# Optimization experiments

Measured on AMD Instinct MI355X. Metric: run time of the kernel, lower is better.

## Reference

```python
import jax, jax.numpy as jnp
import numpy as np

PRED, TOTAL, ITEM = 100000, 120000, 100000
NUI = PRED + ITEM            # nodes in user2item / reverse-consumption graphs
NODES = TOTAL + ITEM         # embedding table rows
EMB = 64
EPS = 1e-5


def _gatv2(src, dst, x, Wl, bl, Wr, br, attn, n):
    """DGL GATv2Conv (1 head), activation=leaky_relu(0.01)."""
    fs = x @ Wl + bl                                   # fc_src
    fd = x @ Wr + br                                   # fc_dst
    e = jax.nn.leaky_relu(fs[src] + fd[dst], 0.2) @ attn   # [E_edges]
    m = jax.ops.segment_max(e, dst, n)                 # per-dst max (stable softmax)
    ex = jnp.exp(e - m[dst])
    denom = jax.ops.segment_sum(ex, dst, n)
    alpha = ex / denom[dst]                            # edge softmax over in-edges
    out = jax.ops.segment_sum(alpha[:, None] * fs[src], dst, n)
    return jax.nn.leaky_relu(out, 0.01)


def _bn(x, g, b):
    mu = jnp.mean(x, 0)
    var = jnp.var(x, 0)
    return (x - mu) * jax.lax.rsqrt(var + EPS) * g + b


def _mlp(x, W, b, g, beta):
    # Linear -> BatchNorm1d (train mode, batch stats) -> LeakyReLU(0.01)
    return jax.nn.leaky_relu(_bn(x @ W + b, g, beta), 0.01)


def _cheb(src, dst, x, W, b, lam, n):
    """ChebConv order-3: h = sum_k T_k(Lhat) x @ W_k + b, leaky_relu."""
    deg = jnp.clip(jax.ops.segment_sum(jnp.ones_like(dst, jnp.float32), dst, n), 1.0)
    dinv = jax.lax.rsqrt(deg)
    norm = dinv[src] * dinv[dst]                       # D^-1/2 A D^-1/2 edge weight

    def lhat(v):  # (2/lam)(I - Ahat) v - v
        av = jax.ops.segment_sum(norm[:, None] * v[src], dst, n)
        return (2.0 / lam) * (v - av) - v

    T0 = x
    T1 = lhat(T0)
    T2 = 2.0 * lhat(T1) - T0
    return jax.nn.leaky_relu(T0 @ W[0] + T1 @ W[1] + T2 @ W[2] + b, 0.01)


def setup_inputs() -> dict:
    key = jax.random.key(0)
    ks = jax.random.split(key, 24)
    ri = lambda k, n, hi: jax.random.randint(k, (n,), 0, hi, dtype=jnp.int32)
    rn = lambda k, shp, s=0.1: jax.random.normal(k, shp, jnp.float32) * s
    return {
        "emb": rn(ks[0], (NODES, EMB), 1.0),
        "bn0_g": jnp.ones((EMB,), jnp.float32),
        "bn0_b": jnp.zeros((EMB,), jnp.float32),
        "gat_Wl": rn(ks[1], (5, EMB, EMB)),
        "gat_bl": jnp.zeros((5, EMB), jnp.float32),
        "gat_Wr": rn(ks[2], (5, EMB, EMB)),
        "gat_br": jnp.zeros((5, EMB), jnp.float32),
        "gat_attn": rn(ks[3], (5, EMB)),
        "cheb_W": rn(ks[4], (3, EMB, EMB)),
        "cheb_b": jnp.zeros((EMB,), jnp.float32),
        "mlp_W": rn(ks[5], (5, 2 * EMB, EMB)),
        "mlp_b": jnp.zeros((5, EMB), jnp.float32),
        "mlp_g": jnp.ones((5, EMB), jnp.float32),
        "mlp_beta": jnp.zeros((5, EMB), jnp.float32),
        "lambda_max": jnp.array([2.0], jnp.float32),
        "u2i_src": ri(ks[6], 1500000, NUI),
        "u2i_dst": ri(ks[7], 1500000, NUI),
        "rc_src": ri(ks[8], 1500000, NUI),
        "rc_dst": ri(ks[9], 1500000, NUI),
        "i2u_src": ri(ks[10], 1000000, PRED),
        "i2u_dst": ri(ks[11], 1000000, PRED),
        "i2u_ids": jnp.arange(PRED, dtype=jnp.int32),
        "sn_src": ri(ks[12], 1000000, PRED),
        "sn_dst": ri(ks[13], 1000000, PRED),
        "snn_src": ri(ks[14], 1500000, TOTAL),
        "snn_dst": ri(ks[15], 1500000, TOTAL),
    }


def reference(emb, bn0_g, bn0_b, gat_Wl, gat_bl, gat_Wr, gat_br, gat_attn,
              cheb_W, cheb_b, mlp_W, mlp_b, mlp_g, mlp_beta, lambda_max,
              u2i_src, u2i_dst, rc_src, rc_dst, i2u_src, i2u_dst, i2u_ids,
              sn_src, sn_dst, snn_src, snn_dst):
    gat = lambda i, src, dst, x, n: _gatv2(src, dst, x, gat_Wl[i], gat_bl[i],
                                           gat_Wr[i], gat_br[i], gat_attn[i], n)
    mlp = lambda i, x: _mlp(x, mlp_W[i], mlp_b[i], mlp_g[i], mlp_beta[i])

    e = _bn(emb, bn0_g, bn0_b)                        # embedding_BN over all nodes
    pred_u = e[:PRED]
    total_u = e[:TOTAL]
    item_e = e[-ITEM:]
    uie = jnp.concatenate([pred_u, item_e], axis=0)   # [NUI, EMB]

    # --- spatial attention: item influence branch ---
    u2i_emb = gat(0, u2i_src, u2i_dst, uie, NUI)
    iie = gat(1, rc_src, rc_dst, u2i_emb, NUI)[:PRED]

    # --- spatial attention: social item branch ---
    su = uie[i2u_ids]                                 # embedding[_ID]
    i2u_emb = gat(2, i2u_src, i2u_dst, su, PRED)
    soc = uie[:PRED]                                  # embedding[social_g.nodes()]
    mask = (jnp.sum(i2u_emb, axis=1) != 0)[:, None]
    soc = soc.at[i2u_ids].set(jnp.where(mask, i2u_emb, soc[i2u_ids]))
    sie = gat(3, sn_src, sn_dst, soc, PRED)

    user_item_embed = mlp(0, jnp.concatenate([iie, sie], axis=1))

    # --- spectral attention ---
    lam = lambda_max[0]
    h = _cheb(snn_src, snn_dst, total_u, cheb_W, cheb_b, lam, TOTAL)
    h = _cheb(snn_src, snn_dst, h, cheb_W, cheb_b, lam, TOTAL)
    user_social_embed = gat(4, snn_src, snn_dst, h, TOTAL)[:PRED]

    # --- mutualistic layer ---
    h_uP = mlp(1, jnp.concatenate([user_item_embed, pred_u], axis=1))
    h_uS = mlp(2, jnp.concatenate([user_social_embed, pred_u], axis=1))
    h_m = h_uP * h_uS
    h_mP = jnp.concatenate([h_m * jax.nn.softmax(h_uP, axis=1), h_uP], axis=1)
    h_mS = jnp.concatenate([h_m * jax.nn.softmax(h_uS, axis=1), h_uS], axis=1)

    # --- prediction layer ---
    h_new_P = mlp(3, h_mP)
    h_new_S = mlp(4, h_mS)
    return (h_new_P, h_new_S)
```

## Files before the change

kernel.cpp:

```cpp
#include <hip/hip_runtime.h>
#include <math.h>

static const int PRED  = 100000;
static const int TOTAL = 120000;
static const int ITEM  = 100000;
static const int NUI   = PRED + ITEM;
static const int NODES = TOTAL + ITEM;
#define BN_EPS 1e-5f

__device__ inline float lrelu(float v, float s) { return v > 0.f ? v : s * v; }

__global__ void k_bn_stats(const float* __restrict__ x, int n, float* __restrict__ sums) {
  __shared__ float ls[256], ls2[256];
  int t = threadIdx.x;
  int col = t & 63;
  float s = 0.f, s2 = 0.f;
  for (int r = blockIdx.x * 4 + (t >> 6); r < n; r += gridDim.x * 4) {
    float v = x[(size_t)r * 64 + col];
    s += v; s2 += v * v;
  }
  ls[t] = s; ls2[t] = s2;
  __syncthreads();
  if (t < 64) {
    atomicAdd(&sums[t],      ls[t] + ls[t + 64] + ls[t + 128] + ls[t + 192]);
    atomicAdd(&sums[64 + t], ls2[t] + ls2[t + 64] + ls2[t + 128] + ls2[t + 192]);
  }
}

__global__ void k_bn_apply(const float* __restrict__ x, float* __restrict__ y,
                           const float* __restrict__ sums,
                           const float* __restrict__ g, const float* __restrict__ b,
                           int n, int relu) {
  size_t tot4 = (size_t)n * 16;
  size_t i = (size_t)blockIdx.x * blockDim.x + threadIdx.x;
  size_t st = (size_t)gridDim.x * blockDim.x;
  float inv_n = 1.f / (float)n;
  const float4* x4 = (const float4*)x;
  float4* y4 = (float4*)y;
  for (; i < tot4; i += st) {
    int c4 = (int)(i & 15) * 4;
    float4 v = x4[i];
    float4 o;
    #pragma unroll
    for (int j = 0; j < 4; ++j) {
      int c = c4 + j;
      float mean = sums[c] * inv_n;
      float var = fmaxf(sums[64 + c] * inv_n - mean * mean, 0.f);
      float vv = (j == 0) ? v.x : (j == 1) ? v.y : (j == 2) ? v.z : v.w;
      float oo = (vv - mean) * rsqrtf(var + BN_EPS) * g[c] + b[c];
      if (relu) oo = lrelu(oo, 0.01f);
      if (j == 0) o.x = oo; else if (j == 1) o.y = oo; else if (j == 2) o.z = oo; else o.w = oo;
    }
    y4[i] = o;
  }
}

__global__ void k_bn0_apply(const float* __restrict__ x, float* __restrict__ e_tot,
                            float* __restrict__ uie, const float* __restrict__ sums,
                            const float* __restrict__ g, const float* __restrict__ b) {
  size_t tot4 = (size_t)NODES * 16;
  size_t i = (size_t)blockIdx.x * blockDim.x + threadIdx.x;
  size_t st = (size_t)gridDim.x * blockDim.x;
  float inv_n = 1.f / (float)NODES;
  const float4* x4 = (const float4*)x;
  float4* e4 = (float4*)e_tot;
  float4* u4 = (float4*)uie;
  for (; i < tot4; i += st) {
    int c4 = (int)(i & 15) * 4;
    size_t row = i >> 4;
    float4 v = x4[i];
    float4 o;
    #pragma unroll
    for (int j = 0; j < 4; ++j) {
      int c = c4 + j;
      float mean = sums[c] * inv_n;
      float var = fmaxf(sums[64 + c] * inv_n - mean * mean, 0.f);
      float vv = (j == 0) ? v.x : (j == 1) ? v.y : (j == 2) ? v.z : v.w;
      float oo = (vv - mean) * rsqrtf(var + BN_EPS) * g[c] + b[c];
      if (j == 0) o.x = oo; else if (j == 1) o.y = oo; else if (j == 2) o.z = oo; else o.w = oo;
    }
    if (row < (size_t)TOTAL) e4[i] = o;
    else u4[((row - TOTAL) + PRED) * 16 + (i & 15)] = o;
    if (row < (size_t)PRED) u4[i] = o;
  }
}

__global__ __launch_bounds__(256) void k_gemm_dual(const float* __restrict__ A,
    const float* __restrict__ Wl, const float* __restrict__ bl,
    const float* __restrict__ Wr, const float* __restrict__ br,
    float* __restrict__ FS, float* __restrict__ FD, int n) {
  __shared__ float As[128][65];
  __shared__ float Ws[64][68];
  int t = threadIdx.x;
  int row0 = blockIdx.x * 128;
  for (int i = t; i < 2048; i += 256) {
    int r = i >> 4, c = (i & 15) * 4, gr = row0 + r;
    float4 a;
    if (gr < n) a = *(const float4*)&A[(size_t)gr * 64 + c];
    else { a.x = a.y = a.z = a.w = 0.f; }
    As[r][c] = a.x; As[r][c + 1] = a.y; As[r][c + 2] = a.z; As[r][c + 3] = a.w;
  }
  int cg = (t & 7) * 8;
  int rg = (t >> 3) * 4;
  for (int s = 0; s < 2; ++s) {
    const float* Wm = s ? Wr : Wl;
    const float* bias = s ? br : bl;
    __syncthreads();
    for (int i = t; i < 4096; i += 256) Ws[i >> 6][i & 63] = Wm[i];
    __syncthreads();
    float bb[8];
    *(float4*)&bb[0] = *(const float4*)&bias[cg];
    *(float4*)&bb[4] = *(const float4*)&bias[cg + 4];
    float acc[4][8];
    #pragma unroll
    for (int i = 0; i < 4; ++i)
      #pragma unroll
      for (int j = 0; j < 8; ++j) acc[i][j] = bb[j];
    for (int k = 0; k < 64; ++k) {
      float w[8], a[4];
      *(float4*)&w[0] = *(const float4*)&Ws[k][cg];
      *(float4*)&w[4] = *(const float4*)&Ws[k][cg + 4];
      #pragma unroll
      for (int i = 0; i < 4; ++i) a[i] = As[rg + i][k];
      #pragma unroll
      for (int i = 0; i < 4; ++i)
        #pragma unroll
        for (int j = 0; j < 8; ++j)
          acc[i][j] += a[i] * w[j];
    }
    float* C = s ? FD : FS;
    #pragma unroll
    for (int i = 0; i < 4; ++i) {
      int gr = row0 + rg + i;
      if (gr < n) {
        float4 o0, o1;
        o0.x = acc[i][0]; o0.y = acc[i][1]; o0.z = acc[i][2]; o0.w = acc[i][3];
        o1.x = acc[i][4]; o1.y = acc[i][5]; o1.z = acc[i][6]; o1.w = acc[i][7];
        *(float4*)&FS[0];
        *(float4*)&C[(size_t)gr * 64 + cg] = o0;
        *(float4*)&C[(size_t)gr * 64 + cg + 4] = o1;
      }
    }
  }
}

__global__ __launch_bounds__(256) void k_gemm_cat(const float* __restrict__ A1,
    const float* __restrict__ A2, const float* __restrict__ A3,
    const float* __restrict__ Wm, const float* __restrict__ bias,
    float* __restrict__ C, int n, int nseg, int relu, float* __restrict__ stats) {
  __shared__ float As[128][65];
  __shared__ float Ws[64][68];
  __shared__ float st[128];
  int t = threadIdx.x;
  int row0 = blockIdx.x * 128;
  int cg = (t & 7) * 8;
  int rg = (t >> 3) * 4;
  float bb[8];
  *(float4*)&bb[0] = *(const float4*)&bias[cg];
  *(float4*)&bb[4] = *(const float4*)&bias[cg + 4];
  float acc[4][8];
  #pragma unroll
  for (int i = 0; i < 4; ++i)
    #pragma unroll
    for (int j = 0; j < 8; ++j) acc[i][j] = bb[j];
  for (int s = 0; s < nseg; ++s) {
    const float* A = (s == 0) ? A1 : (s == 1) ? A2 : A3;
    __syncthreads();
    for (int i = t; i < 4096; i += 256) Ws[i >> 6][i & 63] = Wm[s * 4096 + i];
    for (int i = t; i < 2048; i += 256) {
      int r = i >> 4, c = (i & 15) * 4, gr = row0 + r;
      float4 a;
      if (gr < n) a = *(const float4*)&A[(size_t)gr * 64 + c];
      else { a.x = a.y = a.z = a.w = 0.f; }
      As[r][c] = a.x; As[r][c + 1] = a.y; As[r][c + 2] = a.z; As[r][c + 3] = a.w;
    }
    __syncthreads();
    for (int k = 0; k < 64; ++k) {
      float w[8], a[4];
      *(float4*)&w[0] = *(const float4*)&Ws[k][cg];
      *(float4*)&w[4] = *(const float4*)&Ws[k][cg + 4];
      #pragma unroll
      for (int i = 0; i < 4; ++i) a[i] = As[rg + i][k];
      #pragma unroll
      for (int i = 0; i < 4; ++i)
        #pragma unroll
        for (int j = 0; j < 8; ++j)
          acc[i][j] += a[i] * w[j];
    }
  }
  float csum[8], csq[8];
  #pragma unroll
  for (int j = 0; j < 8; ++j) { csum[j] = 0.f; csq[j] = 0.f; }
  #pragma unroll
  for (int i = 0; i < 4; ++i) {
    int gr = row0 + rg + i;
    if (gr < n) {
      #pragma unroll
      for (int j = 0; j < 8; ++j) {
        float o = acc[i][j];
        if (relu) o = lrelu(o, 0.01f);
        acc[i][j] = o;
        csum[j] += o;
        csq[j] += o * o;
      }
      float4 o0, o1;
      o0.x = acc[i][0]; o0.y = acc[i][1]; o0.z = acc[i][2]; o0.w = acc[i][3];
      o1.x = acc[i][4]; o1.y = acc[i][5]; o1.z = acc[i][6]; o1.w = acc[i][7];
      *(float4*)&C[(size_t)gr * 64 + cg] = o0;
      *(float4*)&C[(size_t)gr * 64 + cg + 4] = o1;
    }
  }
  if (stats) {
    __syncthreads();
    if (t < 128) st[t] = 0.f;
    __syncthreads();
    #pragma unroll
    for (int j = 0; j < 8; ++j) {
      atomicAdd(&st[cg + j], csum[j]);
      atomicAdd(&st[64 + cg + j], csq[j]);
    }
    __syncthreads();
    if (t < 128) atomicAdd(&stats[t], st[t]);
  }
}

__global__ __launch_bounds__(512) void k_bhist(const int* __restrict__ dst, int* __restrict__ M,
                                               int E, int nbuck, int chunk) {
  __shared__ int h[1600];
  int t = threadIdx.x, b = blockIdx.x;
  for (int k = t; k < nbuck; k += 512) h[k] = 0;
  __syncthreads();
  int beg = b * chunk, end = min(E, beg + chunk);
  for (int i = beg + t; i < end; i += 512) atomicAdd(&h[dst[i] >> 7], 1);
  __syncthreads();
  for (int k = t; k < nbuck; k += 512) M[k * 64 + b] = h[k];
}

__global__ void k_scan_part(const int* __restrict__ counts, int* __restrict__ bsums, int n) {
  __shared__ int sh[256];
  int t = threadIdx.x;
  int i = blockIdx.x * 256 + t;
  sh[t] = (i < n) ? counts[i] : 0;
  __syncthreads();
  for (int o = 128; o; o >>= 1) {
    if (t < o) sh[t] += sh[t + o];
    __syncthreads();
  }
  if (t == 0) bsums[blockIdx.x] = sh[0];
}

__global__ void k_scan_tops(int* __restrict__ bsums, int nb) {
  __shared__ int sh[256];
  int t = threadIdx.x;
  int carry = 0;
  for (int base = 0; base < nb; base += 256) {
    int i = base + t;
    int v = (i < nb) ? bsums[i] : 0;
    __syncthreads();
    sh[t] = v;
    __syncthreads();
    for (int o = 1; o < 256; o <<= 1) {
      int tv = (t >= o) ? sh[t - o] : 0;
      __syncthreads();
      sh[t] += tv;
      __syncthreads();
    }
    int incl = sh[t];
    int total = sh[255];
    if (i < nb) bsums[i] = incl - v + carry;
    carry += total;
  }
}

__global__ void k_scan_apply_ip(int* __restrict__ cnts, const int* __restrict__ bsums, int n) {
  __shared__ int sh[256];
  int t = threadIdx.x;
  int i = blockIdx.x * 256 + t;
  int v = (i < n) ? cnts[i] : 0;
  sh[t] = v;
  __syncthreads();
  for (int o = 1; o < 256; o <<= 1) {
    int tv = (t >= o) ? sh[t - o] : 0;
    __syncthreads();
    sh[t] += tv;
    __syncthreads();
  }
  if (i < n) cnts[i] = sh[t] - v + bsums[blockIdx.x];
}

__global__ __launch_bounds__(512) void k_bscatter(const int* __restrict__ src, const int* __restrict__ dst,
                                                  const int* __restrict__ M, unsigned int* __restrict__ tmp,
                                                  int E, int nbuck, int chunk) {
  __shared__ int cur[1600];
  int t = threadIdx.x, b = blockIdx.x;
  for (int k = t; k < nbuck; k += 512) cur[k] = M[k * 64 + b];
  __syncthreads();
  int beg = b * chunk, end = min(E, beg + chunk);
  for (int i = beg + t; i < end; i += 512) {
    int d = dst[i];
    int pos = atomicAdd(&cur[d >> 7], 1);
    tmp[pos] = ((unsigned int)(d & 127) << 25) | (unsigned int)src[i];
  }
}

__global__ __launch_bounds__(256) void k_bfinal(const unsigned int* __restrict__ tmp,
                                                const int* __restrict__ M,
                                                int* __restrict__ offs, int* __restrict__ csr,
                                                int E, int nbuck, int n,
                                                float* __restrict__ dinvOut) {
  __shared__ int h[128];
  int t = threadIdx.x, k = blockIdx.x;
  int base = M[k * 64];
  int next = (k + 1 < nbuck) ? M[(k + 1) * 64] : E;
  if (t < 128) h[t] = 0;
  __syncthreads();
  for (int i = base + t; i < next; i += 256) atomicAdd(&h[tmp[i] >> 25], 1);
  __syncthreads();
  if (t == 0) { int s = 0; for (int j = 0; j < 128; ++j) { int c = h[j]; h[j] = s; s += c; } }
  __syncthreads();
  int r0 = k << 7;
  int hstart = 0, hnext = 0;
  if (t < 128) {
    hstart = h[t];
    hnext = (t < 127) ? h[t + 1] : (next - base);
  }
  if (t < 128 && r0 + t < n) {
    offs[r0 + t] = base + hstart;
    if (dinvOut) dinvOut[r0 + t] = rsqrtf(fmaxf((float)(hnext - hstart), 1.f));
  }
  if (k == nbuck - 1 && t == 0) offs[n] = E;
  __syncthreads();
  for (int i = base + t; i < next; i += 256) {
    unsigned int v = tmp[i];
    int rl = (int)(v >> 25);
    int pos = base + atomicAdd(&h[rl], 1);
    csr[pos] = (int)(v & 0x01FFFFFFu);
  }
}

__global__ __launch_bounds__(256) void k_gat_fused(const float* __restrict__ fs,
                                                   const float* __restrict__ fd,
                                                   const float* __restrict__ attn,
                                                   const int* __restrict__ offs,
                                                   const int* __restrict__ csr_src,
                                                   const float* __restrict__ sel,
                                                   float* __restrict__ out, int n) {
  int lane = threadIdx.x & 63;
  int g  = lane >> 4;
  int li = lane & 15;
  int c4 = li * 4;
  int wid = (blockIdx.x * blockDim.x + threadIdx.x) >> 6;
  int nw = (gridDim.x * blockDim.x) >> 6;
  float4 ak = *(const float4*)&attn[c4];
  for (int r = wid; r < n; r += nw) {
    int beg = offs[r], end = offs[r + 1];
    float4 fdv = *(const float4*)&fd[(size_t)r * 64 + c4];
    float den = 0.f;
    float4 acc; acc.x = acc.y = acc.z = acc.w = 0.f;
    int e0 = beg + g;
    int s = (e0 < end) ? csr_src[e0] : 0;
    float4 f = *(const float4*)&fs[(size_t)s * 64 + c4];
    for (int e4 = beg; e4 < end; e4 += 4) {
      bool act = (e4 + g) < end;
      int en = e4 + 4 + g;
      int sn = (en < end) ? csr_src[en] : 0;
      float4 fn = *(const float4*)&fs[(size_t)sn * 64 + c4];
      float w = ak.x * lrelu(f.x + fdv.x, 0.2f)
              + ak.y * lrelu(f.y + fdv.y, 0.2f)
              + ak.z * lrelu(f.z + fdv.z, 0.2f)
              + ak.w * lrelu(f.w + fdv.w, 0.2f);
      w += __shfl_xor(w, 1);
      w += __shfl_xor(w, 2);
      w += __shfl_xor(w, 4);
      w += __shfl_xor(w, 8);
      float p = act ? __expf(w) : 0.f;
      den += p;
      acc.x += p * f.x;
      acc.y += p * f.y;
      acc.z += p * f.z;
      acc.w += p * f.w;
      s = sn; f = fn;
    }
    #pragma unroll
    for (int o = 16; o < 64; o <<= 1) {
      den   += __shfl_xor(den, o);
      acc.x += __shfl_xor(acc.x, o);
      acc.y += __shfl_xor(acc.y, o);
      acc.z += __shfl_xor(acc.z, o);
      acc.w += __shfl_xor(acc.w, o);
    }
    if (g == 0) {
      float inv = (end > beg) ? 1.f / den : 0.f;
      float4 o4;
      o4.x = lrelu(acc.x * inv, 0.01f);
      o4.y = lrelu(acc.y * inv, 0.01f);
      o4.z = lrelu(acc.z * inv, 0.01f);
      o4.w = lrelu(acc.w * inv, 0.01f);
      if (sel) {
        float rs = o4.x + o4.y + o4.z + o4.w;
        rs += __shfl_xor(rs, 1);
        rs += __shfl_xor(rs, 2);
        rs += __shfl_xor(rs, 4);
        rs += __shfl_xor(rs, 8);
        if (rs == 0.f) o4 = *(const float4*)&sel[(size_t)r * 64 + c4];
      }
      *(float4*)&out[(size_t)r * 64 + c4] = o4;
    }
  }
}

__global__ __launch_bounds__(256) void k_cheb_fused(const float* __restrict__ v,
                                                    const float* __restrict__ t0,
                                                    const float* __restrict__ dinv,
                                                    const int* __restrict__ offs,
                                                    const int* __restrict__ csr_src,
                                                    float* __restrict__ out,
                                                    const float* __restrict__ lamf,
                                                    int n, int mode) {
  int lane = threadIdx.x & 63;
  int g  = lane >> 4;
  int li = lane & 15;
  int c4 = li * 4;
  int wid = (blockIdx.x * blockDim.x + threadIdx.x) >> 6;
  int nw = (gridDim.x * blockDim.x) >> 6;
  float cc = 2.f / lamf[0];
  for (int r = wid; r < n; r += nw) {
    int beg = offs[r], end = offs[r + 1];
    float dr = dinv[r];
    float4 acc; acc.x = acc.y = acc.z = acc.w = 0.f;
    int e0 = beg + g;
    int s = (e0 < end) ? csr_src[e0] : 0;
    float ds = dinv[s];
    float4 f = *(const float4*)&v[(size_t)s * 64 + c4];
    for (int e4 = beg; e4 < end; e4 += 4) {
      bool act = (e4 + g) < end;
      int en = e4 + 4 + g;
      int sn = (en < end) ? csr_src[en] : 0;
      float dsn = dinv[sn];
      float4 fn = *(const float4*)&v[(size_t)sn * 64 + c4];
      float ns = act ? ds * dr : 0.f;
      acc.x += ns * f.x;
      acc.y += ns * f.y;
      acc.z += ns * f.z;
      acc.w += ns * f.w;
      s = sn; ds = dsn; f = fn;
    }
    #pragma unroll
    for (int o = 16; o < 64; o <<= 1) {
      acc.x += __shfl_xor(acc.x, o);
      acc.y += __shfl_xor(acc.y, o);
      acc.z += __shfl_xor(acc.z, o);
      acc.w += __shfl_xor(acc.w, o);
    }
    if (g == 0) {
      float4 vr = *(const float4*)&v[(size_t)r * 64 + c4];
      float4 o4;
      o4.x = cc * (vr.x - acc.x) - vr.x;
      o4.y = cc * (vr.y - acc.y) - vr.y;
      o4.z = cc * (vr.z - acc.z) - vr.z;
      o4.w = cc * (vr.w - acc.w) - vr.w;
      if (mode == 2) {
        float4 t = *(const float4*)&t0[(size_t)r * 64 + c4];
        o4.x = 2.f * o4.x - t.x;
        o4.y = 2.f * o4.y - t.y;
        o4.z = 2.f * o4.z - t.z;
        o4.w = 2.f * o4.w - t.w;
      }
      *(float4*)&out[(size_t)r * 64 + c4] = o4;
    }
  }
}

__global__ void k_softmax_mul(const float* __restrict__ a, const float* __restrict__ b,
                              float* __restrict__ out, int n) {
  int lane = threadIdx.x & 63;
  int wid = (blockIdx.x * blockDim.x + threadIdx.x) >> 6;
  int nw = (gridDim.x * blockDim.x) >> 6;
  for (int r = wid; r < n; r += nw) {
    size_t idx = (size_t)r * 64 + lane;
    float av = a[idx];
    float mx = av;
    for (int o = 32; o; o >>= 1) mx = fmaxf(mx, __shfl_xor(mx, o));
    float e = expf(av - mx);
    float s = e;
    for (int o = 32; o; o >>= 1) s += __shfl_xor(s, o);
    out[idx] = av * b[idx] * (e / s);
  }
}

extern "C" void kernel_launch(void* const* d_in, const int* in_sizes, int n_in,
                              void* d_out, int out_size, void* d_ws, size_t ws_size,
                              hipStream_t stream) {
  const float* emb      = (const float*)d_in[0];
  const float* bn0_g    = (const float*)d_in[1];
  const float* bn0_b    = (const float*)d_in[2];
  const float* gat_Wl   = (const float*)d_in[3];
  const float* gat_bl   = (const float*)d_in[4];
  const float* gat_Wr   = (const float*)d_in[5];
  const float* gat_br   = (const float*)d_in[6];
  const float* gat_attn = (const float*)d_in[7];
  const float* cheb_W   = (const float*)d_in[8];
  const float* cheb_b   = (const float*)d_in[9];
  const float* mlp_W    = (const float*)d_in[10];
  const float* mlp_b    = (const float*)d_in[11];
  const float* mlp_g    = (const float*)d_in[12];
  const float* mlp_beta = (const float*)d_in[13];
  const float* lam      = (const float*)d_in[14];
  const int* u2i_src = (const int*)d_in[15];
  const int* u2i_dst = (const int*)d_in[16];
  const int* rc_src  = (const int*)d_in[17];
  const int* rc_dst  = (const int*)d_in[18];
  const int* i2u_src = (const int*)d_in[19];
  const int* i2u_dst = (const int*)d_in[20];
  const int* sn_src  = (const int*)d_in[22];
  const int* sn_dst  = (const int*)d_in[23];
  const int* snn_src = (const int*)d_in[24];
  const int* snn_dst = (const int*)d_in[25];
  int E_u2i = in_sizes[15], E_rc = in_sizes[17], E_i2u = in_sizes[19];
  int E_sn = in_sizes[22], E_snn = in_sizes[24];

  float* Wp = (float*)d_ws;
  size_t off = 0;
  auto alloc = [&](size_t nf) { float* p = Wp + off; off += nf; return p; };
  float* e_tot = alloc((size_t)TOTAL * 64);
  float* POOL  = alloc((size_t)600000 * 64);
  int*   csr_src = (int*)alloc(1500000);
  int*   offs    = (int*)alloc(200064);
  float* spare   = alloc(200064);
  int*   bsums   = (int*)alloc(1024);
  float* dinv  = alloc(TOTAL);
  float* sums  = alloc(896);

  auto R = [&](size_t row) { return POOL + row * 64; };
  unsigned int* tmp_e = (unsigned int*)R(520000);
  int*          Mbuf  = (int*)R(545000);
  (void)spare;

  float* outP = (float*)d_out;
  float* outS = outP + (size_t)PRED * 64;

  auto build_csr = [&](const int* src, const int* dst, int E, int n, float* dv) {
    int nbuck = (n + 127) >> 7;
    int chunk = (E + 63) / 64;
    int L = nbuck * 64;
    int NB = (L + 255) / 256;
    k_bhist<<<64, 512, 0, stream>>>(dst, Mbuf, E, nbuck, chunk);
    k_scan_part<<<NB, 256, 0, stream>>>(Mbuf, bsums, L);
    k_scan_tops<<<1, 256, 0, stream>>>(bsums, NB);
    k_scan_apply_ip<<<NB, 256, 0, stream>>>(Mbuf, bsums, L);
    k_bscatter<<<64, 512, 0, stream>>>(src, dst, Mbuf, tmp_e, E, nbuck, chunk);
    k_bfinal<<<nbuck, 256, 0, stream>>>(tmp_e, Mbuf, offs, csr_src, E, nbuck, n, dv);
  };
  auto gat = [&](int i, const float* fs, const float* fd, int n, const float* sel, float* out) {
    k_gat_fused<<<(n + 3) / 4, 256, 0, stream>>>(fs, fd, gat_attn + i * 64, offs, csr_src, sel, out, n);
  };
  auto gat_gemms = [&](int i, const float* A, float* fs, float* fd, int n) {
    k_gemm_dual<<<(n + 127) / 128, 256, 0, stream>>>(A, gat_Wl + i * 4096, gat_bl + i * 64,
                                                     gat_Wr + i * 4096, gat_br + i * 64, fs, fd, n);
  };
  auto cat2s = [&](const float* A1, const float* A2, const float* Wm, const float* bias,
                   float* C, int n, int slot) {
    k_gemm_cat<<<(n + 127) / 128, 256, 0, stream>>>(A1, A2, nullptr, Wm, bias, C, n, 2, 0,
                                                    sums + slot * 128);
  };

  hipMemsetAsync(sums, 0, 896 * 4, stream);

  k_bn_stats<<<512, 256, 0, stream>>>(emb, NODES, sums);
  k_bn0_apply<<<2048, 256, 0, stream>>>(emb, e_tot, R(0), sums, bn0_g, bn0_b);

  build_csr(u2i_src, u2i_dst, E_u2i, NUI, nullptr);
  gat_gemms(0, R(0), R(200000), R(400000), NUI);
  gat(0, R(200000), R(400000), NUI, nullptr, R(0));

  build_csr(rc_src, rc_dst, E_rc, NUI, nullptr);
  gat_gemms(1, R(0), R(200000), R(400000), NUI);
  gat(1, R(200000), R(400000), NUI, nullptr, R(0));

  build_csr(i2u_src, i2u_dst, E_i2u, PRED, nullptr);
  gat_gemms(2, e_tot, R(200000), R(300000), PRED);
  gat(2, R(200000), R(300000), PRED, e_tot, R(400000));

  build_csr(sn_src, sn_dst, E_sn, PRED, nullptr);
  gat_gemms(3, R(400000), R(200000), R(500000), PRED);
  gat(3, R(200000), R(500000), PRED, nullptr, R(300000));

  cat2s(R(0), R(300000), mlp_W + 0 * 8192, mlp_b + 0, R(100000), PRED, 1);
  k_bn_apply<<<2048, 256, 0, stream>>>(R(100000), R(0), sums + 128, mlp_g + 0, mlp_beta + 0, PRED, 1);

  build_csr(snn_src, snn_dst, E_snn, TOTAL, dinv);

  auto cheb = [&](const float* T0, float* T1, float* T2, float* outC) {
    k_cheb_fused<<<(TOTAL + 3) / 4, 256, 0, stream>>>(T0, T0, dinv, offs, csr_src, T1, lam, TOTAL, 1);
    k_cheb_fused<<<(TOTAL + 3) / 4, 256, 0, stream>>>(T1, T0, dinv, offs, csr_src, T2, lam, TOTAL, 2);
    k_gemm_cat<<<(TOTAL + 127) / 128, 256, 0, stream>>>(T0, T1, T2, cheb_W, cheb_b, outC, TOTAL, 3, 1, nullptr);
  };
  cheb(e_tot, R(100000), R(220000), R(340000));
  cheb(R(340000), R(100000), R(220000), R(460000));

  gat_gemms(4, R(460000), R(100000), R(220000), TOTAL);
  gat(4, R(100000), R(220000), TOTAL, nullptr, R(460000));

  cat2s(R(0), e_tot, mlp_W + 1 * 8192, mlp_b + 64, R(100000), PRED, 2);
  k_bn_apply<<<2048, 256, 0, stream>>>(R(100000), R(100000), sums + 256, mlp_g + 64, mlp_beta + 64, PRED, 1);

  cat2s(R(460000), e_tot, mlp_W + 2 * 8192, mlp_b + 128, R(200000), PRED, 3);
  k_bn_apply<<<2048, 256, 0, stream>>>(R(200000), R(200000), sums + 384, mlp_g + 128, mlp_beta + 128, PRED, 1);

  k_softmax_mul<<<2048, 256, 0, stream>>>(R(100000), R(200000), R(300000), PRED);
  cat2s(R(300000), R(100000), mlp_W + 3 * 8192, mlp_b + 192, R(400000), PRED, 4);
  k_bn_apply<<<2048, 256, 0, stream>>>(R(400000), outP, sums + 512, mlp_g + 192, mlp_beta + 192, PRED, 1);

  k_softmax_mul<<<2048, 256, 0, stream>>>(R(200000), R(100000), R(300000), PRED);
  cat2s(R(300000), R(200000), mlp_W + 4 * 8192, mlp_b + 256, R(400000), PRED, 5);
  k_bn_apply<<<2048, 256, 0, stream>>>(R(400000), outS, sums + 640, mlp_g + 256, mlp_beta + 256, PRED, 1);
}
```

Before: 2.049 ms.

## Halve GEMM row tiles, single-kernel CSR scan, fuse BN+softmax into final MLPs

GEMM kernels now process 64 rows per block instead of 128, giving more blocks and fewer accumulator registers per thread. The three-kernel prefix scan in CSR construction becomes one single-block wave-shuffle scan kernel. BN-apply and softmax-multiply for the mutualistic layer are folded into a new fused MLP kernel that recomputes normalization while staging inputs into shared memory, which removes intermediate buffers and launches. Buffer assignments are reshuffled to match. The trade-offs are redundant BN recomputation in both final MLPs and a serial single-block scan.

After: 2.382 ms. 1.16x slower.

```diff
diff --git a/kernel.cpp b/kernel.cpp
--- a/kernel.cpp
+++ b/kernel.cpp
@@ -8,7 +8,7 @@
 static const int NODES = TOTAL + ITEM;
 #define BN_EPS 1e-5f
 
-__device__ inline float lrelu(float v, float s) { return v > 0.f ? v : s * v; }
+__device__ inline float lrelu(float v, float s) { return fmaxf(v, s * v); }
 
 __global__ void k_bn_stats(const float* __restrict__ x, int n, float* __restrict__ sums) {
   __shared__ float ls[256], ls2[256];
@@ -89,11 +89,11 @@
     const float* __restrict__ Wl, const float* __restrict__ bl,
     const float* __restrict__ Wr, const float* __restrict__ br,
     float* __restrict__ FS, float* __restrict__ FD, int n) {
-  __shared__ float As[128][65];
+  __shared__ float As[64][65];
   __shared__ float Ws[64][68];
   int t = threadIdx.x;
-  int row0 = blockIdx.x * 128;
-  for (int i = t; i < 2048; i += 256) {
+  int row0 = blockIdx.x * 64;
+  for (int i = t; i < 1024; i += 256) {
     int r = i >> 4, c = (i & 15) * 4, gr = row0 + r;
     float4 a;
     if (gr < n) a = *(const float4*)&A[(size_t)gr * 64 + c];
@@ -101,7 +101,7 @@
     As[r][c] = a.x; As[r][c + 1] = a.y; As[r][c + 2] = a.z; As[r][c + 3] = a.w;
   }
   int cg = (t & 7) * 8;
-  int rg = (t >> 3) * 4;
+  int rg = (t >> 3) * 2;
   for (int s = 0; s < 2; ++s) {
     const float* Wm = s ? Wr : Wl;
     const float* bias = s ? br : bl;
@@ -111,32 +111,31 @@
     float bb[8];
     *(float4*)&bb[0] = *(const float4*)&bias[cg];
     *(float4*)&bb[4] = *(const float4*)&bias[cg + 4];
-    float acc[4][8];
-    #pragma unroll
-    for (int i = 0; i < 4; ++i)
+    float acc[2][8];
+    #pragma unroll
+    for (int i = 0; i < 2; ++i)
       #pragma unroll
       for (int j = 0; j < 8; ++j) acc[i][j] = bb[j];
     for (int k = 0; k < 64; ++k) {
-      float w[8], a[4];
+      float w[8], a[2];
       *(float4*)&w[0] = *(const float4*)&Ws[k][cg];
       *(float4*)&w[4] = *(const float4*)&Ws[k][cg + 4];
       #pragma unroll
-      for (int i = 0; i < 4; ++i) a[i] = As[rg + i][k];
-      #pragma unroll
-      for (int i = 0; i < 4; ++i)
+      for (int i = 0; i < 2; ++i) a[i] = As[rg + i][k];
+      #pragma unroll
+      for (int i = 0; i < 2; ++i)
         #pragma unroll
         for (int j = 0; j < 8; ++j)
           acc[i][j] += a[i] * w[j];
     }
     float* C = s ? FD : FS;
     #pragma unroll
-    for (int i = 0; i < 4; ++i) {
+    for (int i = 0; i < 2; ++i) {
       int gr = row0 + rg + i;
       if (gr < n) {
         float4 o0, o1;
         o0.x = acc[i][0]; o0.y = acc[i][1]; o0.z = acc[i][2]; o0.w = acc[i][3];
         o1.x = acc[i][4]; o1.y = acc[i][5]; o1.z = acc[i][6]; o1.w = acc[i][7];
-        *(float4*)&FS[0];
         *(float4*)&C[(size_t)gr * 64 + cg] = o0;
         *(float4*)&C[(size_t)gr * 64 + cg + 4] = o1;
       }
@@ -148,26 +147,26 @@
     const float* __restrict__ A2, const float* __restrict__ A3,
     const float* __restrict__ Wm, const float* __restrict__ bias,
     float* __restrict__ C, int n, int nseg, int relu, float* __restrict__ stats) {
-  __shared__ float As[128][65];
+  __shared__ float As[64][65];
   __shared__ float Ws[64][68];
   __shared__ float st[128];
   int t = threadIdx.x;
-  int row0 = blockIdx.x * 128;
+  int row0 = blockIdx.x * 64;
   int cg = (t & 7) * 8;
-  int rg = (t >> 3) * 4;
+  int rg = (t >> 3) * 2;
   float bb[8];
   *(float4*)&bb[0] = *(const float4*)&bias[cg];
   *(float4*)&bb[4] = *(const float4*)&bias[cg + 4];
-  float acc[4][8];
+  float acc[2][8];
   #pragma unroll
-  for (int i = 0; i < 4; ++i)
+  for (int i = 0; i < 2; ++i)
     #pragma unroll
     for (int j = 0; j < 8; ++j) acc[i][j] = bb[j];
   for (int s = 0; s < nseg; ++s) {
     const float* A = (s == 0) ? A1 : (s == 1) ? A2 : A3;
     __syncthreads();
     for (int i = t; i < 4096; i += 256) Ws[i >> 6][i & 63] = Wm[s * 4096 + i];
-    for (int i = t; i < 2048; i += 256) {
+    for (int i = t; i < 1024; i += 256) {
       int r = i >> 4, c = (i & 15) * 4, gr = row0 + r;
       float4 a;
       if (gr < n) a = *(const float4*)&A[(size_t)gr * 64 + c];
@@ -176,13 +175,13 @@
     }
     __syncthreads();
     for (int k = 0; k < 64; ++k) {
-      float w[8], a[4];
+      float w[8], a[2];
       *(float4*)&w[0] = *(const float4*)&Ws[k][cg];
       *(float4*)&w[4] = *(const float4*)&Ws[k][cg + 4];
       #pragma unroll
-      for (int i = 0; i < 4; ++i) a[i] = As[rg + i][k];
-      #pragma unroll
-      for (int i = 0; i < 4; ++i)
+      for (int i = 0; i < 2; ++i) a[i] = As[rg + i][k];
+      #pragma unroll
+      for (int i = 0; i < 2; ++i)
         #pragma unroll
         for (int j = 0; j < 8; ++j)
           acc[i][j] += a[i] * w[j];
@@ -192,7 +191,7 @@
   #pragma unroll
   for (int j = 0; j < 8; ++j) { csum[j] = 0.f; csq[j] = 0.f; }
   #pragma unroll
-  for (int i = 0; i < 4; ++i) {
+  for (int i = 0; i < 2; ++i) {
     int gr = row0 + rg + i;
     if (gr < n) {
       #pragma unroll
@@ -224,6 +223,120 @@
   }
 }
 
+__global__ __launch_bounds__(256) void k_mlp_final(const float* __restrict__ rawA,
+    const float* __restrict__ rawB,
+    const float* __restrict__ sA, const float* __restrict__ gA, const float* __restrict__ bA,
+    const float* __restrict__ sB, const float* __restrict__ gB, const float* __restrict__ bB,
+    float invn, const float* __restrict__ Wm, const float* __restrict__ bias,
+    float* __restrict__ C, int n, float* __restrict__ stats) {
+  __shared__ float As[64][65];
+  __shared__ float Ws[64][68];
+  __shared__ float st[128];
+  int t = threadIdx.x;
+  int row0 = blockIdx.x * 64;
+  int cg = (t & 7) * 8;
+  int rg = (t >> 3) * 2;
+  float bb[8];
+  *(float4*)&bb[0] = *(const float4*)&bias[cg];
+  *(float4*)&bb[4] = *(const float4*)&bias[cg + 4];
+  float acc[2][8];
+  #pragma unroll
+  for (int i = 0; i < 2; ++i)
+    #pragma unroll
+    for (int j = 0; j < 8; ++j) acc[i][j] = bb[j];
+  for (int s = 0; s < 2; ++s) {
+    __syncthreads();
+    for (int i = t; i < 4096; i += 256) Ws[i >> 6][i & 63] = Wm[s * 4096 + i];
+    for (int i = t; i < 1024; i += 256) {
+      int r = i >> 4, c = (i & 15) * 4, gr = row0 + r;
+      float av[4], out4[4];
+      #pragma unroll
+      for (int j = 0; j < 4; ++j) {
+        int ch = c + j;
+        float va = (gr < n) ? rawA[(size_t)gr * 64 + ch] : 0.f;
+        float mean = sA[ch] * invn;
+        float var = fmaxf(sA[64 + ch] * invn - mean * mean, 0.f);
+        float aa = lrelu((va - mean) * rsqrtf(var + BN_EPS) * gA[ch] + bA[ch], 0.01f);
+        av[j] = (gr < n) ? aa : 0.f;
+      }
+      if (s == 1) {
+        out4[0] = av[0]; out4[1] = av[1]; out4[2] = av[2]; out4[3] = av[3];
+      } else {
+        float bv[4];
+        #pragma unroll
+        for (int j = 0; j < 4; ++j) {
+          int ch = c + j;
+          float vb = (gr < n) ? rawB[(size_t)gr * 64 + ch] : 0.f;
+          float mean = sB[ch] * invn;
+          float var = fmaxf(sB[64 + ch] * invn - mean * mean, 0.f);
+          float bbv = lrelu((vb - mean) * rsqrtf(var + BN_EPS) * gB[ch] + bB[ch], 0.01f);
+          bv[j] = (gr < n) ? bbv : 0.f;
+        }
+        float mx = fmaxf(fmaxf(av[0], av[1]), fmaxf(av[2], av[3]));
+        mx = fmaxf(mx, __shfl_xor(mx, 1));
+        mx = fmaxf(mx, __shfl_xor(mx, 2));
+        mx = fmaxf(mx, __shfl_xor(mx, 4));
+        mx = fmaxf(mx, __shfl_xor(mx, 8));
+        float e[4];
+        float ss = 0.f;
+        #pragma unroll
+        for (int j = 0; j < 4; ++j) { e[j] = expf(av[j] - mx); ss += e[j]; }
+        ss += __shfl_xor(ss, 1);
+        ss += __shfl_xor(ss, 2);
+        ss += __shfl_xor(ss, 4);
+        ss += __shfl_xor(ss, 8);
+        float inv = 1.f / ss;
+        #pragma unroll
+        for (int j = 0; j < 4; ++j) out4[j] = av[j] * bv[j] * e[j] * inv;
+      }
+      As[r][c] = out4[0]; As[r][c + 1] = out4[1]; As[r][c + 2] = out4[2]; As[r][c + 3] = out4[3];
+    }
+    __syncthreads();
+    for (int k = 0; k < 64; ++k) {
+      float w[8], a[2];
+      *(float4*)&w[0] = *(const float4*)&Ws[k][cg];
+      *(float4*)&w[4] = *(const float4*)&Ws[k][cg + 4];
+      #pragma unroll
+      for (int i = 0; i < 2; ++i) a[i] = As[rg + i][k];
+      #pragma unroll
+      for (int i = 0; i < 2; ++i)
+        #pragma unroll
+        for (int j = 0; j < 8; ++j)
+          acc[i][j] += a[i] * w[j];
+    }
+  }
+  float csum[8], csq[8];
+  #pragma unroll
+  for (int j = 0; j < 8; ++j) { csum[j] = 0.f; csq[j] = 0.f; }
+  #pragma unroll
+  for (int i = 0; i < 2; ++i) {
+    int gr = row0 + rg + i;
+    if (gr < n) {
+      #pragma unroll
+      for (int j = 0; j < 8; ++j) {
+        float o = acc[i][j];
+        csum[j] += o;
+        csq[j] += o * o;
+      }
+      float4 o0, o1;
+      o0.x = acc[i][0]; o0.y = acc[i][1]; o0.z = acc[i][2]; o0.w = acc[i][3];
+      o1.x = acc[i][4]; o1.y = acc[i][5]; o1.z = acc[i][6]; o1.w = acc[i][7];
+      *(float4*)&C[(size_t)gr * 64 + cg] = o0;
+      *(float4*)&C[(size_t)gr * 64 + cg + 4] = o1;
+    }
+  }
+  __syncthreads();
+  if (t < 128) st[t] = 0.f;
+  __syncthreads();
+  #pragma unroll
+  for (int j = 0; j < 8; ++j) {
+    atomicAdd(&st[cg + j], csum[j]);
+    atomicAdd(&st[64 + cg + j], csq[j]);
+  }
+  __syncthreads();
+  if (t < 128) atomicAdd(&stats[t], st[t]);
+}
+
 __global__ __launch_bounds__(512) void k_bhist(const int* __restrict__ dst, int* __restrict__ M,
                                                int E, int nbuck, int chunk) {
   __shared__ int h[1600];
@@ -236,56 +349,33 @@
   for (int k = t; k < nbuck; k += 512) M[k * 64 + b] = h[k];
 }
 
-__global__ void k_scan_part(const int* __restrict__ counts, int* __restrict__ bsums, int n) {
-  __shared__ int sh[256];
-  int t = threadIdx.x;
-  int i = blockIdx.x * 256 + t;
-  sh[t] = (i < n) ? counts[i] : 0;
-  __syncthreads();
-  for (int o = 128; o; o >>= 1) {
-    if (t < o) sh[t] += sh[t + o];
-    __syncthreads();
-  }
-  if (t == 0) bsums[blockIdx.x] = sh[0];
-}
-
-__global__ void k_scan_tops(int* __restrict__ bsums, int nb) {
-  __shared__ int sh[256];
-  int t = threadIdx.x;
-  int carry = 0;
-  for (int base = 0; base < nb; base += 256) {
+__global__ __launch_bounds__(1024) void k_scan_one(int* __restrict__ cnts, int L) {
+  __shared__ int wsum[16];
+  __shared__ int carry_s;
+  int t = threadIdx.x, lane = t & 63, w = t >> 6;
+  if (t == 0) carry_s = 0;
+  __syncthreads();
+  for (int base = 0; base < L; base += 1024) {
     int i = base + t;
-    int v = (i < nb) ? bsums[i] : 0;
-    __syncthreads();
-    sh[t] = v;
-    __syncthreads();
-    for (int o = 1; o < 256; o <<= 1) {
-      int tv = (t >= o) ? sh[t - o] : 0;
-      __syncthreads();
-      sh[t] += tv;
-      __syncthreads();
-    }
-    int incl = sh[t];
-    int total = sh[255];
-    if (i < nb) bsums[i] = incl - v + carry;
-    carry += total;
-  }
-}
-
-__global__ void k_scan_apply_ip(int* __restrict__ cnts, const int* __restrict__ bsums, int n) {
-  __shared__ int sh[256];
-  int t = threadIdx.x;
-  int i = blockIdx.x * 256 + t;
-  int v = (i < n) ? cnts[i] : 0;
-  sh[t] = v;
-  __syncthreads();
-  for (int o = 1; o < 256; o <<= 1) {
-    int tv = (t >= o) ? sh[t - o] : 0;
-    __syncthreads();
-    sh[t] += tv;
-    __syncthreads();
-  }
-  if (i < n) cnts[i] = sh[t] - v + bsums[blockIdx.x];
+    int v = (i < L) ? cnts[i] : 0;
+    int x = v;
+    #pragma unroll
+    for (int o = 1; o < 64; o <<= 1) {
+      int y = __shfl_up(x, o);
+      if (lane >= o) x += y;
+    }
+    if (lane == 63) wsum[w] = x;
+    __syncthreads();
+    int carry = carry_s;
+    int wadd = 0;
+    #pragma unroll
+    for (int j = 0; j < 16; ++j) { int sv = wsum[j]; if (j < w) wadd += sv; }
+    int incl = x + wadd + carry;
+    if (i < L) cnts[i] = incl - v;
+    __syncthreads();
+    if (t == 1023) carry_s = incl;
+    __syncthreads();
+  }
 }
 
 __global__ __launch_bounds__(512) void k_bscatter(const int* __restrict__ src, const int* __restrict__ dst,
@@ -471,23 +561,6 @@
   }
 }
 
-__global__ void k_softmax_mul(const float* __restrict__ a, const float* __restrict__ b,
-                              float* __restrict__ out, int n) {
-  int lane = threadIdx.x & 63;
-  int wid = (blockIdx.x * blockDim.x + threadIdx.x) >> 6;
-  int nw = (gridDim.x * blockDim.x) >> 6;
-  for (int r = wid; r < n; r += nw) {
-    size_t idx = (size_t)r * 64 + lane;
-    float av = a[idx];
-    float mx = av;
-    for (int o = 32; o; o >>= 1) mx = fmaxf(mx, __shfl_xor(mx, o));
-    float e = expf(av - mx);
-    float s = e;
-    for (int o = 32; o; o >>= 1) s += __shfl_xor(s, o);
-    out[idx] = av * b[idx] * (e / s);
-  }
-}
-
 extern "C" void kernel_launch(void* const* d_in, const int* in_sizes, int n_in,
                               void* d_out, int out_size, void* d_ws, size_t ws_size,
                               hipStream_t stream) {
@@ -530,24 +603,21 @@
   int*   bsums   = (int*)alloc(1024);
   float* dinv  = alloc(TOTAL);
   float* sums  = alloc(896);
-
   auto R = [&](size_t row) { return POOL + row * 64; };
   unsigned int* tmp_e = (unsigned int*)R(520000);
   int*          Mbuf  = (int*)R(545000);
-  (void)spare;
+  (void)spare; (void)bsums;
 
   float* outP = (float*)d_out;
   float* outS = outP + (size_t)PRED * 64;
+  float invP = 1.f / (float)PRED;
 
   auto build_csr = [&](const int* src, const int* dst, int E, int n, float* dv) {
     int nbuck = (n + 127) >> 7;
     int chunk = (E + 63) / 64;
     int L = nbuck * 64;
-    int NB = (L + 255) / 256;
     k_bhist<<<64, 512, 0, stream>>>(dst, Mbuf, E, nbuck, chunk);
-    k_scan_part<<<NB, 256, 0, stream>>>(Mbuf, bsums, L);
-    k_scan_tops<<<1, 256, 0, stream>>>(bsums, NB);
-    k_scan_apply_ip<<<NB, 256, 0, stream>>>(Mbuf, bsums, L);
+    k_scan_one<<<1, 1024, 0, stream>>>(Mbuf, L);
     k_bscatter<<<64, 512, 0, stream>>>(src, dst, Mbuf, tmp_e, E, nbuck, chunk);
     k_bfinal<<<nbuck, 256, 0, stream>>>(tmp_e, Mbuf, offs, csr_src, E, nbuck, n, dv);
   };
@@ -555,13 +625,13 @@
     k_gat_fused<<<(n + 3) / 4, 256, 0, stream>>>(fs, fd, gat_attn + i * 64, offs, csr_src, sel, out, n);
   };
   auto gat_gemms = [&](int i, const float* A, float* fs, float* fd, int n) {
-    k_gemm_dual<<<(n + 127) / 128, 256, 0, stream>>>(A, gat_Wl + i * 4096, gat_bl + i * 64,
-                                                     gat_Wr + i * 4096, gat_br + i * 64, fs, fd, n);
+    k_gemm_dual<<<(n + 63) / 64, 256, 0, stream>>>(A, gat_Wl + i * 4096, gat_bl + i * 64,
+                                                   gat_Wr + i * 4096, gat_br + i * 64, fs, fd, n);
   };
   auto cat2s = [&](const float* A1, const float* A2, const float* Wm, const float* bias,
                    float* C, int n, int slot) {
-    k_gemm_cat<<<(n + 127) / 128, 256, 0, stream>>>(A1, A2, nullptr, Wm, bias, C, n, 2, 0,
-                                                    sums + slot * 128);
+    k_gemm_cat<<<(n + 63) / 64, 256, 0, stream>>>(A1, A2, nullptr, Wm, bias, C, n, 2, 0,
+                                                  sums + slot * 128);
   };
 
   hipMemsetAsync(sums, 0, 896 * 4, stream);
@@ -590,28 +660,31 @@
 
   build_csr(snn_src, snn_dst, E_snn, TOTAL, dinv);
 
-  auto cheb = [&](const float* T0, float* T1, float* T2, float* outC) {
-    k_cheb_fused<<<(TOTAL + 3) / 4, 256, 0, stream>>>(T0, T0, dinv, offs, csr_src, T1, lam, TOTAL, 1);
-    k_cheb_fused<<<(TOTAL + 3) / 4, 256, 0, stream>>>(T1, T0, dinv, offs, csr_src, T2, lam, TOTAL, 2);
-    k_gemm_cat<<<(TOTAL + 127) / 128, 256, 0, stream>>>(T0, T1, T2, cheb_W, cheb_b, outC, TOTAL, 3, 1, nullptr);
-  };
-  cheb(e_tot, R(100000), R(220000), R(340000));
-  cheb(R(340000), R(100000), R(220000), R(460000));
-
-  gat_gemms(4, R(460000), R(100000), R(220000), TOTAL);
-  gat(4, R(100000), R(220000), TOTAL, nullptr, R(460000));
-
-  cat2s(R(0), e_tot, mlp_W + 1 * 8192, mlp_b + 64, R(100000), PRED, 2);
-  k_bn_apply<<<2048, 256, 0, stream>>>(R(100000), R(100000), sums + 256, mlp_g + 64, mlp_beta + 64, PRED, 1);
-
-  cat2s(R(460000), e_tot, mlp_W + 2 * 8192, mlp_b + 128, R(200000), PRED, 3);
-  k_bn_apply<<<2048, 256, 0, stream>>>(R(200000), R(200000), sums + 384, mlp_g + 128, mlp_beta + 128, PRED, 1);
-
-  k_softmax_mul<<<2048, 256, 0, stream>>>(R(100000), R(200000), R(300000), PRED);
-  cat2s(R(300000), R(100000), mlp_W + 3 * 8192, mlp_b + 192, R(400000), PRED, 4);
+  k_cheb_fused<<<(TOTAL + 3) / 4, 256, 0, stream>>>(e_tot, e_tot, dinv, offs, csr_src, R(220000), lam, TOTAL, 1);
+  k_cheb_fused<<<(TOTAL + 3) / 4, 256, 0, stream>>>(R(220000), e_tot, dinv, offs, csr_src, R(460000), lam, TOTAL, 2);
+  k_gemm_cat<<<(TOTAL + 63) / 64, 256, 0, stream>>>(e_tot, R(220000), R(460000), cheb_W, cheb_b,
+                                                    R(340000), TOTAL, 3, 1, nullptr);
+  k_cheb_fused<<<(TOTAL + 3) / 4, 256, 0, stream>>>(R(340000), R(340000), dinv, offs, csr_src, R(220000), lam, TOTAL, 1);
+  k_cheb_fused<<<(TOTAL + 3) / 4, 256, 0, stream>>>(R(220000), R(340000), dinv, offs, csr_src, R(460000), lam, TOTAL, 2);
+  k_gemm_cat<<<(TOTAL + 63) / 64, 256, 0, stream>>>(R(340000), R(220000), R(460000), cheb_W, cheb_b,
+                                                    R(100000), TOTAL, 3, 1, nullptr);
+
+  gat_gemms(4, R(100000), R(220000), R(340000), TOTAL);
+  gat(4, R(220000), R(340000), TOTAL, nullptr, R(460000));
+
+  cat2s(R(0), e_tot, mlp_W + 1 * 8192, mlp_b + 64, R(200000), PRED, 2);
+
+  cat2s(R(460000), e_tot, mlp_W + 2 * 8192, mlp_b + 128, R(300000), PRED, 3);
+
+  k_mlp_final<<<(PRED + 63) / 64, 256, 0, stream>>>(R(200000), R(300000),
+      sums + 256, mlp_g + 64, mlp_beta + 64,
+      sums + 384, mlp_g + 128, mlp_beta + 128, invP,
+      mlp_W + 3 * 8192, mlp_b + 192, R(400000), PRED, sums + 512);
   k_bn_apply<<<2048, 256, 0, stream>>>(R(400000), outP, sums + 512, mlp_g + 192, mlp_beta + 192, PRED, 1);
 
-  k_softmax_mul<<<2048, 256, 0, stream>>>(R(200000), R(100000), R(300000), PRED);
-  cat2s(R(300000), R(200000), mlp_W + 4 * 8192, mlp_b + 256, R(400000), PRED, 5);
-  k_bn_apply<<<2048, 256, 0, stream>>>(R(400000), outS, sums + 640, mlp_g + 256, mlp_beta + 256, PRED, 1);
-}
+  k_mlp_final<<<(PRED + 63) / 64, 256, 0, stream>>>(R(300000), R(200000),
+      sums + 384, mlp_g + 128, mlp_beta + 128,
+      sums + 256, mlp_g + 64, mlp_beta + 64, invP,
+      mlp_W + 4 * 8192, mlp_b + 256, R(100000), PRED, sums + 640);
+  k_bn_apply<<<2048, 256, 0, stream>>>(R(100000), outS, sums + 640, mlp_g + 256, mlp_beta + 256, PRED, 1);
+}
```
